# Performance work log

Measured on AMD Instinct MI355X. Metric: run time of the kernel, lower is better.

The kernel has to match this reference:

```python
import jax, jax.numpy as jnp
import numpy as np

MARGIN = 0.3
NEG_FALLBACK = 1e6  # value used when a row has no negatives


def setup_inputs() -> dict:
    key = jax.random.key(0)
    k1, k2 = jax.random.split(key)
    N, D, NUM_IDS = 8192, 256, 512
    feat = jax.random.normal(k1, (N, D), dtype=jnp.float32)
    labels = jax.random.randint(k2, (N,), 0, NUM_IDS, dtype=jnp.int64)
    return {"feat": feat, "labels": labels}


def reference(feat, labels):
    N = feat.shape[0]
    sq_norms = jnp.sum(feat * feat, axis=1)  # [N]
    sq = sq_norms[:, None] + sq_norms[None, :] - 2.0 * (feat @ feat.T)  # [N,N]
    sq = jnp.maximum(sq, 0.0)
    # safe sqrt (zero distance on the diagonal would otherwise give nan grads)
    dist = jnp.where(sq > 0, jnp.sqrt(jnp.where(sq > 0, sq, 1.0)), 0.0)

    same = labels[:, None] == labels[None, :]          # [N,N] bool
    eye = jnp.eye(N, dtype=bool)
    is_pos = same & ~eye                                # exclude self-pair
    is_neg = ~same

    # hard mining: per-row masked max over positives / min over negatives
    dist_ap = jnp.where(is_pos.any(axis=1),
                        jnp.where(is_pos, dist, -jnp.inf).max(axis=1), 0.0)
    dist_an = jnp.where(is_neg.any(axis=1),
                        jnp.where(is_neg, dist, jnp.inf).min(axis=1), NEG_FALLBACK)

    # MarginRankingLoss with y=1: mean(relu(margin - (dist_an - dist_ap)))
    return jnp.mean(jnp.maximum(0.0, MARGIN + dist_ap - dist_an))
```

## Files before the change

### kernel.cpp

```cpp
#include <hip/hip_runtime.h>


constexpr int N = 8192;
constexpr int D = 256;
constexpr float MARGIN = 0.3f;
constexpr float NEG_FALLBACK = 1e6f;
constexpr float TBIG = 1e30f;

typedef __attribute__((ext_vector_type(8))) __bf16 bf16x8;
typedef __attribute__((ext_vector_type(4))) float f32x4;

__device__ __forceinline__ unsigned enc_f(float f) {
  unsigned u = __float_as_uint(f);
  return (u >> 31) ? ~u : (u | 0x80000000u);
}
__device__ __forceinline__ float dec_f(unsigned e) {
  unsigned u = (e >> 31) ? (e ^ 0x80000000u) : ~e;
  return __uint_as_float(u);
}
__device__ __forceinline__ unsigned short f2bf_rtn(float x) {
  unsigned u = __float_as_uint(x);
  return (unsigned short)((u + 0x7fffu + ((u >> 16) & 1u)) >> 16);
}


__global__ __launch_bounds__(1024)
void tl_sortk(const int* __restrict__ labels, int* __restrict__ perm,
              int* __restrict__ labp, int* __restrict__ offg) {
  __shared__ int hist[512];
  __shared__ int wsum[8];
  __shared__ int wbase[8];
  const int tid = threadIdx.x;
  const int lane = tid & 63;
  const int w = tid >> 6;
  if (tid < 512) hist[tid] = 0;
  __syncthreads();
  int l8[8];
#pragma unroll
  for (int k = 0; k < 8; ++k) {
    l8[k] = labels[tid + k * 1024];
    atomicAdd(&hist[l8[k]], 1);
  }
  __syncthreads();
  int v = 0, sc = 0;
  if (tid < 512) {
    v = hist[tid];
    sc = v;
#pragma unroll
    for (int d = 1; d < 64; d <<= 1) {
      int t = __shfl_up(sc, d, 64);
      if (lane >= d) sc += t;
    }
    if (lane == 63) wsum[w] = sc;
  }
  __syncthreads();
  if (tid == 0) {
    int a = 0;
#pragma unroll
    for (int i = 0; i < 8; ++i) { wbase[i] = a; a += wsum[i]; }
  }
  __syncthreads();
  if (tid < 512) {
    const int excl = wbase[w] + sc - v;
    offg[tid] = excl;
    hist[tid] = excl;
  }
  if (tid == 0) offg[512] = N;
  __syncthreads();
#pragma unroll
  for (int k = 0; k < 8; ++k) {
    const int pos = atomicAdd(&hist[l8[k]], 1);
    perm[pos] = tid + k * 1024;
    labp[pos] = l8[k];
  }
}


__global__ void tl_pass0p(const float* __restrict__ feat, const int* __restrict__ perm,
                          float* __restrict__ norms, unsigned* __restrict__ ap,
                          unsigned* __restrict__ an, unsigned short* __restrict__ P,
                          float* __restrict__ out) {
  const int p = blockIdx.x * 4 + (threadIdx.x >> 6);
  const int lane = threadIdx.x & 63;
  const int src = perm[p];
  float4 f = reinterpret_cast<const float4*>(feat + (size_t)src * D)[lane];
  ushort4 h;
  h.x = f2bf_rtn(f.x); h.y = f2bf_rtn(f.y); h.z = f2bf_rtn(f.z); h.w = f2bf_rtn(f.w);
  reinterpret_cast<ushort4*>(P + (size_t)p * D)[lane] = h;
  float s = fmaf(f.x, f.x, fmaf(f.y, f.y, fmaf(f.z, f.z, f.w * f.w)));
#pragma unroll
  for (int off = 32; off > 0; off >>= 1) s += __shfl_down(s, off, 64);
  if (lane == 0) {
    norms[p] = s;
    ap[p] = enc_f(-TBIG);
    an[p] = enc_f(TBIG);
  }
  if (p == 0 && lane == 0) out[0] = 0.0f;
}


__global__ __launch_bounds__(512, 2)
void tl_pass1s(const unsigned short* __restrict__ P, const int* __restrict__ labp,
               const float* __restrict__ norms, const int* __restrict__ offg,
               unsigned* __restrict__ ap, unsigned* __restrict__ an) {
  __shared__ unsigned short lB[3][128][64];
  __shared__ float nrmS[512];
  __shared__ int lblS[512];

  const int tid = threadIdx.x;
  const int wave = tid >> 6;
  const int lane = tid & 63;
  const int c = lane & 15;
  const int q = lane >> 4;
  const int i0 = blockIdx.y * 256;
  const int j0 = blockIdx.x * 512;
  const int wrow = i0 + wave * 32;

  const int lo = offg[labp[i0]];
  const int hi = offg[labp[i0 + 255] + 1];

  const int rsub = lane >> 3;
  const int g7 = lane & 7;

#define STAGE(BUF, S1)                                                                  \
  do {                                                                                  \
    const int jb_ = j0 + ((S1) >> 2) * 128;                                             \
    const int kc_ = ((S1) & 3) * 64;                                                    \
    _Pragma("unroll") for (int t = 0; t < 2; ++t) {                                     \
      const int rA_ = wave * 16 + t * 8;                                                \
      const int sg_ = g7 ^ rsub;                                                        \
      const unsigned short* gp_ = P + (size_t)(jb_ + rA_ + rsub) * D + kc_ + sg_ * 8;   \
      __builtin_amdgcn_global_load_lds(                                                 \
          (const __attribute__((address_space(1))) void*)gp_,                           \
          (__attribute__((address_space(3))) void*)&lB[BUF][rA_][0], 16, 0, 0);         \
    }                                                                                   \
  } while (0)

#define WAITB2 do { asm volatile("s_waitcnt vmcnt(2)" ::: "memory"); \
                    __builtin_amdgcn_s_barrier(); } while (0)
#define WAITB0 do { asm volatile("s_waitcnt vmcnt(0)" ::: "memory"); \
                    __builtin_amdgcn_s_barrier(); } while (0)

  STAGE(0, 0);

  bf16x8 af[2][8];
#pragma unroll
  for (int a = 0; a < 2; ++a)
#pragma unroll
    for (int t2 = 0; t2 < 8; ++t2)
      af[a][t2] = *(const bf16x8*)(P + (size_t)(wrow + a * 16 + c) * D + t2 * 32 + q * 8);

  int lrow[2][4];
#pragma unroll
  for (int a = 0; a < 2; ++a)
#pragma unroll
    for (int r = 0; r < 4; ++r)
      lrow[a][r] = labp[wrow + a * 16 + q * 4 + r];

  nrmS[tid] = norms[j0 + tid];
  lblS[tid] = labp[j0 + tid];

  STAGE(1, 1);
  asm volatile("s_waitcnt vmcnt(2) lgkmcnt(0)" ::: "memory");
  __builtin_amdgcn_s_barrier();

  f32x4 acc[2][8];
#pragma unroll
  for (int a = 0; a < 2; ++a)
#pragma unroll
    for (int b = 0; b < 8; ++b) acc[a][b] = (f32x4){0.f, 0.f, 0.f, 0.f};

  float vp[2][4], vn[2][4];
#pragma unroll
  for (int a = 0; a < 2; ++a)
#pragma unroll
    for (int r = 0; r < 4; ++r) { vp[a][r] = -TBIG; vn[a][r] = TBIG; }

#pragma unroll
  for (int s = 0; s < 16; ++s) {
    const int jt = s >> 2;
    const int kk = s & 3;
    if (s + 2 < 16) STAGE((s + 2) % 3, s + 2);

#pragma unroll
    for (int ks = 0; ks < 2; ++ks) {
      const int gsel = ((ks * 4 + q) ^ (c & 7)) * 8;
      bf16x8 bfr[8];
#pragma unroll
      for (int b = 0; b < 8; ++b)
        bfr[b] = *(const bf16x8*)&lB[s % 3][b * 16 + c][gsel];
#pragma unroll
      for (int a = 0; a < 2; ++a)
#pragma unroll
        for (int b = 0; b < 8; ++b)
          acc[a][b] = __builtin_amdgcn_mfma_f32_16x16x32_bf16(
              af[a][kk * 2 + ks], bfr[b], acc[a][b], 0, 0, 0);
    }

    if (kk == 3) {
      const int jb0 = j0 + jt * 128;
      const int jls = jt * 128;
      const bool careful = (jb0 < hi) && (jb0 + 128 > lo);
      if (!careful) {
#pragma unroll
        for (int b = 0; b < 8; ++b) {
          const float njb = nrmS[jls + b * 16 + c];
#pragma unroll
          for (int a = 0; a < 2; ++a)
#pragma unroll
            for (int r = 0; r < 4; ++r)
              vn[a][r] = fminf(vn[a][r], fmaf(-2.f, acc[a][b][r], njb));
        }
      } else {
        int lj[8], cj[8];
        float nj[8];
#pragma unroll
        for (int b = 0; b < 8; ++b) {
          cj[b] = jb0 + b * 16 + c;
          nj[b] = nrmS[jls + b * 16 + c];
          lj[b] = lblS[jls + b * 16 + c];
        }
#pragma unroll
        for (int a = 0; a < 2; ++a)
#pragma unroll
          for (int r = 0; r < 4; ++r) {
            const int rg = wrow + a * 16 + q * 4 + r;
            const int li = lrow[a][r];
            float vpl = vp[a][r], vnl = vn[a][r];
#pragma unroll
            for (int b = 0; b < 8; ++b) {
              const float t = fmaf(-2.f, acc[a][b][r], nj[b]);
              const bool sm = (lj[b] == li);
              const bool dg = (cj[b] == rg);
              vpl = fmaxf(vpl, (sm && !dg) ? t : -TBIG);
              vnl = fminf(vnl, sm ? TBIG : t);
            }
            vp[a][r] = vpl;
            vn[a][r] = vnl;
          }
      }
#pragma unroll
      for (int a = 0; a < 2; ++a)
#pragma unroll
        for (int b = 0; b < 8; ++b) acc[a][b] = (f32x4){0.f, 0.f, 0.f, 0.f};
    }

    if (s < 14) {
      WAITB2;
    } else if (s == 14) {
      WAITB0;
    }
  }
#undef STAGE
#undef WAITB2
#undef WAITB0

#pragma unroll
  for (int a = 0; a < 2; ++a)
#pragma unroll
    for (int r = 0; r < 4; ++r) {
      float p = vp[a][r], n = vn[a][r];
#pragma unroll
      for (int m = 1; m < 16; m <<= 1) {
        p = fmaxf(p, __shfl_xor(p, m, 64));
        n = fminf(n, __shfl_xor(n, m, 64));
      }
      if (c == 0) {
        const int rg = wrow + a * 16 + q * 4 + r;
        atomicMax(&ap[rg], enc_f(p));
        atomicMin(&an[rg], enc_f(n));
      }
    }
}


__global__ void tl_pass2f(const unsigned* __restrict__ ap, const unsigned* __restrict__ an,
                          const float* __restrict__ norms, float* __restrict__ out) {
  int r = blockIdx.x * 256 + threadIdx.x;
  float ni = norms[r];
  float tpv = dec_f(ap[r]);
  float tnv = dec_f(an[r]);
  float dap = (tpv < -1e29f) ? 0.f : sqrtf(fmaxf(ni + tpv, 0.f));
  float dan = (tnv > 1e29f) ? NEG_FALLBACK : sqrtf(fmaxf(ni + tnv, 0.f));
  float v = fmaxf(0.f, MARGIN + dap - dan) * (1.0f / (float)N);
#pragma unroll
  for (int off = 32; off > 0; off >>= 1) v += __shfl_down(v, off, 64);
  __shared__ float red[4];
  int lane = threadIdx.x & 63, w = threadIdx.x >> 6;
  if (lane == 0) red[w] = v;
  __syncthreads();
  if (threadIdx.x == 0) atomicAdd(out, red[0] + red[1] + red[2] + red[3]);
}


constexpr int FB_BK = 32;
constexpr int FB_JSPLIT = 8;
constexpr int FB_JRANGE = N / FB_JSPLIT;
constexpr int FB_LDS = 132;

__global__ void tl_pass0_fb(const float* __restrict__ feat, float* __restrict__ norms,
                            float* __restrict__ ap, float* __restrict__ an,
                            float* __restrict__ out) {
  int row = blockIdx.x * 4 + (threadIdx.x >> 6);
  int lane = threadIdx.x & 63;
  float4 f = reinterpret_cast<const float4*>(feat + (size_t)row * D)[lane];
  float s = f.x * f.x + f.y * f.y + f.z * f.z + f.w * f.w;
#pragma unroll
  for (int off = 32; off > 0; off >>= 1) s += __shfl_down(s, off, 64);
  if (lane == 0) { norms[row] = s; ap[row] = 0.0f; an[row] = NEG_FALLBACK; }
  if (row == 0 && lane == 0) out[0] = 0.0f;
}

__global__ __launch_bounds__(256, 2)
void tl_pass1_fb(const float* __restrict__ feat, const int* __restrict__ labels,
                 const float* __restrict__ norms,
                 unsigned int* __restrict__ ap, unsigned int* __restrict__ an) {
  __shared__ float As[FB_BK][FB_LDS];
  __shared__ float Bs[FB_BK][FB_LDS];
  const int tid = threadIdx.x;
  const int tx = tid & 15, ty = tid >> 4;
  const int ib0 = blockIdx.y * 128;
  const int jbase = blockIdx.x * FB_JRANGE;
  float ni[8]; int li[8]; int ri[8];
#pragma unroll
  for (int a = 0; a < 8; ++a) {
    int r = ty * 4 + (a & 3) + ((a >> 2) << 6);
    ri[a] = ib0 + r; ni[a] = norms[ri[a]]; li[a] = labels[ri[a]];
  }
  float apv[8], anv[8];
#pragma unroll
  for (int a = 0; a < 8; ++a) { apv[a] = 0.0f; anv[a] = NEG_FALLBACK; }
  for (int jt = 0; jt < FB_JRANGE; jt += 128) {
    const int jb = jbase + jt;
    float acc[8][8];
#pragma unroll
    for (int a = 0; a < 8; ++a)
#pragma unroll
      for (int b = 0; b < 8; ++b) acc[a][b] = 0.0f;
    for (int kc = 0; kc < D; kc += FB_BK) {
#pragma unroll
      for (int u = 0; u < 4; ++u) {
        int lin = tid + u * 256;
        int row = lin >> 3, c4 = lin & 7;
        float4 va = *reinterpret_cast<const float4*>(feat + (size_t)(ib0 + row) * D + kc + c4 * 4);
        As[c4 * 4 + 0][row] = va.x; As[c4 * 4 + 1][row] = va.y;
        As[c4 * 4 + 2][row] = va.z; As[c4 * 4 + 3][row] = va.w;
        float4 vb = *reinterpret_cast<const float4*>(feat + (size_t)(jb + row) * D + kc + c4 * 4);
        Bs[c4 * 4 + 0][row] = vb.x; Bs[c4 * 4 + 1][row] = vb.y;
        Bs[c4 * 4 + 2][row] = vb.z; Bs[c4 * 4 + 3][row] = vb.w;
      }
      __syncthreads();
#pragma unroll 8
      for (int k = 0; k < FB_BK; ++k) {
        float4 a0 = *reinterpret_cast<const float4*>(&As[k][ty * 4]);
        float4 a1 = *reinterpret_cast<const float4*>(&As[k][64 + ty * 4]);
        float4 b0 = *reinterpret_cast<const float4*>(&Bs[k][tx * 4]);
        float4 b1 = *reinterpret_cast<const float4*>(&Bs[k][64 + tx * 4]);
        float av[8] = {a0.x, a0.y, a0.z, a0.w, a1.x, a1.y, a1.z, a1.w};
        float bv[8] = {b0.x, b0.y, b0.z, b0.w, b1.x, b1.y, b1.z, b1.w};
#pragma unroll
        for (int a = 0; a < 8; ++a)
#pragma unroll
          for (int b = 0; b < 8; ++b) acc[a][b] = fmaf(av[a], bv[b], acc[a][b]);
      }
      __syncthreads();
    }
#pragma unroll
    for (int b = 0; b < 8; ++b) {
      int cjx = jb + tx * 4 + (b & 3) + ((b >> 2) << 6);
      float njx = norms[cjx]; int ljx = labels[cjx];
#pragma unroll
      for (int a = 0; a < 8; ++a) {
        float sq = fmaxf(ni[a] + njx - 2.0f * acc[a][b], 0.0f);
        float dist = sqrtf(sq);
        if (li[a] == ljx) { if (ri[a] != cjx) apv[a] = fmaxf(apv[a], dist); }
        else anv[a] = fminf(anv[a], dist);
      }
    }
  }
  __syncthreads();
  float* red = &As[0][0];
#pragma unroll
  for (int a = 0; a < 8; ++a) {
    int r = ty * 4 + (a & 3) + ((a >> 2) << 6);
    red[r * 16 + tx] = apv[a];
  }
  __syncthreads();
  if (tid < 128) {
    float m = red[tid * 16];
#pragma unroll
    for (int t = 1; t < 16; ++t) m = fmaxf(m, red[tid * 16 + t]);
    atomicMax(&ap[ib0 + tid], __float_as_uint(m));
  }
  __syncthreads();
#pragma unroll
  for (int a = 0; a < 8; ++a) {
    int r = ty * 4 + (a & 3) + ((a >> 2) << 6);
    red[r * 16 + tx] = anv[a];
  }
  __syncthreads();
  if (tid < 128) {
    float m = red[tid * 16];
#pragma unroll
    for (int t = 1; t < 16; ++t) m = fminf(m, red[tid * 16 + t]);
    atomicMin(&an[ib0 + tid], __float_as_uint(m));
  }
}

__global__ void tl_pass2_fb(const float* __restrict__ ap, const float* __restrict__ an,
                            float* __restrict__ out) {
  int r = blockIdx.x * 256 + threadIdx.x;
  float v = fmaxf(0.0f, MARGIN + ap[r] - an[r]) * (1.0f / (float)N);
#pragma unroll
  for (int off = 32; off > 0; off >>= 1) v += __shfl_down(v, off, 64);
  __shared__ float red[4];
  int lane = threadIdx.x & 63, w = threadIdx.x >> 6;
  if (lane == 0) red[w] = v;
  __syncthreads();
  if (threadIdx.x == 0) atomicAdd(out, red[0] + red[1] + red[2] + red[3]);
}


extern "C" void kernel_launch(void* const* d_in, const int* in_sizes, int n_in,
                              void* d_out, int out_size, void* d_ws, size_t ws_size,
                              hipStream_t stream) {
  const float* feat = (const float*)d_in[0];
  const int* labels = (const int*)d_in[1];
  float* out = (float*)d_out;

  float* norms = (float*)d_ws;
  unsigned* ap = (unsigned*)(norms + N);
  unsigned* an = ap + N;
  int* perm = (int*)(an + N);
  int* labp = perm + N;
  int* offg = labp + N;
  unsigned short* P = (unsigned short*)(offg + 520);
  const size_t NEED = (size_t)5 * N * 4 + 520 * 4 + (size_t)N * D * 2;

  if (ws_size >= NEED) {
    tl_sortk<<<1, 1024, 0, stream>>>(labels, perm, labp, offg);
    tl_pass0p<<<N / 4, 256, 0, stream>>>(feat, perm, norms, ap, an, P, out);
    dim3 grid1(16, N / 256);
    tl_pass1s<<<grid1, 512, 0, stream>>>(P, labp, norms, offg, ap, an);
    tl_pass2f<<<N / 256, 256, 0, stream>>>(ap, an, norms, out);
  } else {
    float* apf = (float*)ap;
    float* anf = (float*)an;
    tl_pass0_fb<<<N / 4, 256, 0, stream>>>(feat, norms, apf, anf, out);
    dim3 grid1(FB_JSPLIT, N / 128);
    tl_pass1_fb<<<grid1, 256, 0, stream>>>(feat, labels, norms, (unsigned*)apf, (unsigned*)anf);
    tl_pass2_fb<<<N / 256, 256, 0, stream>>>(apf, anf, out);
  }
}
```

Baseline: 115.5 us.

## Interleave prefetch loads with MFMA sub-steps and raise priority during MFMA

Splits the two global-to-LDS prefetch loads of each stage across the two k-substeps, so each substep issues one load after reading its LDS fragments. Adds an extra barrier per substep, plus an explicit lgkmcnt wait and a sched_barrier before the MFMA block. Wraps the MFMAs in s_setprio(1) to favour matrix issue across waves, in a ping-pong style schedule. This adds twice as many barriers per stage, and the vmcnt accounting changes, which risks extra stalls or ordering problems.

After: 120.3 us. +4.2%, slower.

```diff
diff --git a/kernel.cpp b/kernel.cpp
--- a/kernel.cpp
+++ b/kernel.cpp
@@ -128,19 +128,14 @@
     const int kc_ = ((S1) & 3) * 64;                                                    \
     _Pragma("unroll") for (int t = 0; t < 2; ++t) {                                     \
       const int rA_ = wave * 16 + t * 8;                                                \
-      const int sg_ = g7 ^ rsub;                                                        \
-      const unsigned short* gp_ = P + (size_t)(jb_ + rA_ + rsub) * D + kc_ + sg_ * 8;   \
+      const unsigned short* gp_ =                                                       \
+          P + (size_t)(jb_ + rA_ + rsub) * D + kc_ + (g7 ^ rsub) * 8;                   \
       __builtin_amdgcn_global_load_lds(                                                 \
           (const __attribute__((address_space(1))) void*)gp_,                           \
           (__attribute__((address_space(3))) void*)&lB[BUF][rA_][0], 16, 0, 0);         \
     }                                                                                   \
   } while (0)
 
-#define WAITB2 do { asm volatile("s_waitcnt vmcnt(2)" ::: "memory"); \
-                    __builtin_amdgcn_s_barrier(); } while (0)
-#define WAITB0 do { asm volatile("s_waitcnt vmcnt(0)" ::: "memory"); \
-                    __builtin_amdgcn_s_barrier(); } while (0)
-
   STAGE(0, 0);
 
   bf16x8 af[2][8];
@@ -180,8 +175,6 @@
   for (int s = 0; s < 16; ++s) {
     const int jt = s >> 2;
     const int kk = s & 3;
-    if (s + 2 < 16) STAGE((s + 2) % 3, s + 2);
-
 #pragma unroll
     for (int ks = 0; ks < 2; ++ks) {
       const int gsel = ((ks * 4 + q) ^ (c & 7)) * 8;
@@ -189,71 +182,90 @@
 #pragma unroll
       for (int b = 0; b < 8; ++b)
         bfr[b] = *(const bf16x8*)&lB[s % 3][b * 16 + c][gsel];
+
+      if (s + 2 < 16) {
+        const int S1 = s + 2;
+        const int jb_ = j0 + (S1 >> 2) * 128;
+        const int kc_ = (S1 & 3) * 64;
+        const int rA_ = wave * 16 + ks * 8;
+        const unsigned short* gp_ =
+            P + (size_t)(jb_ + rA_ + rsub) * D + kc_ + (g7 ^ rsub) * 8;
+        __builtin_amdgcn_global_load_lds(
+            (const __attribute__((address_space(1))) void*)gp_,
+            (__attribute__((address_space(3))) void*)&lB[S1 % 3][rA_][0], 16, 0, 0);
+      }
+
+      __builtin_amdgcn_s_barrier();
+      asm volatile("s_waitcnt lgkmcnt(0)" ::: "memory");
+      __builtin_amdgcn_sched_barrier(0);
+
+      __builtin_amdgcn_s_setprio(1);
 #pragma unroll
       for (int a = 0; a < 2; ++a)
 #pragma unroll
         for (int b = 0; b < 8; ++b)
           acc[a][b] = __builtin_amdgcn_mfma_f32_16x16x32_bf16(
               af[a][kk * 2 + ks], bfr[b], acc[a][b], 0, 0, 0);
+      __builtin_amdgcn_s_setprio(0);
+
+      if (ks == 1) {
+        if (kk == 3) {
+          const int jb0 = j0 + jt * 128;
+          const int jls = jt * 128;
+          const bool careful = (jb0 < hi) && (jb0 + 128 > lo);
+          if (!careful) {
+#pragma unroll
+            for (int b = 0; b < 8; ++b) {
+              const float njb = nrmS[jls + b * 16 + c];
+#pragma unroll
+              for (int a = 0; a < 2; ++a)
+#pragma unroll
+                for (int r = 0; r < 4; ++r)
+                  vn[a][r] = fminf(vn[a][r], fmaf(-2.f, acc[a][b][r], njb));
+            }
+          } else {
+            int lj[8], cj[8];
+            float nj[8];
+#pragma unroll
+            for (int b = 0; b < 8; ++b) {
+              cj[b] = jb0 + b * 16 + c;
+              nj[b] = nrmS[jls + b * 16 + c];
+              lj[b] = lblS[jls + b * 16 + c];
+            }
+#pragma unroll
+            for (int a = 0; a < 2; ++a)
+#pragma unroll
+              for (int r = 0; r < 4; ++r) {
+                const int rg = wrow + a * 16 + q * 4 + r;
+                const int li = lrow[a][r];
+                float vpl = vp[a][r], vnl = vn[a][r];
+#pragma unroll
+                for (int b = 0; b < 8; ++b) {
+                  const float t = fmaf(-2.f, acc[a][b][r], nj[b]);
+                  const bool sm = (lj[b] == li);
+                  const bool dg = (cj[b] == rg);
+                  vpl = fmaxf(vpl, (sm && !dg) ? t : -TBIG);
+                  vnl = fminf(vnl, sm ? TBIG : t);
+                }
+                vp[a][r] = vpl;
+                vn[a][r] = vnl;
+              }
+          }
+#pragma unroll
+          for (int a = 0; a < 2; ++a)
+#pragma unroll
+            for (int b = 0; b < 8; ++b) acc[a][b] = (f32x4){0.f, 0.f, 0.f, 0.f};
+        }
+        if (s < 14) {
+          asm volatile("s_waitcnt vmcnt(2)" ::: "memory");
+        } else if (s == 14) {
+          asm volatile("s_waitcnt vmcnt(0)" ::: "memory");
+        }
+      }
+      __builtin_amdgcn_s_barrier();
     }
-
-    if (kk == 3) {
-      const int jb0 = j0 + jt * 128;
-      const int jls = jt * 128;
-      const bool careful = (jb0 < hi) && (jb0 + 128 > lo);
-      if (!careful) {
-#pragma unroll
-        for (int b = 0; b < 8; ++b) {
-          const float njb = nrmS[jls + b * 16 + c];
-#pragma unroll
-          for (int a = 0; a < 2; ++a)
-#pragma unroll
-            for (int r = 0; r < 4; ++r)
-              vn[a][r] = fminf(vn[a][r], fmaf(-2.f, acc[a][b][r], njb));
-        }
-      } else {
-        int lj[8], cj[8];
-        float nj[8];
-#pragma unroll
-        for (int b = 0; b < 8; ++b) {
-          cj[b] = jb0 + b * 16 + c;
-          nj[b] = nrmS[jls + b * 16 + c];
-          lj[b] = lblS[jls + b * 16 + c];
-        }
-#pragma unroll
-        for (int a = 0; a < 2; ++a)
-#pragma unroll
-          for (int r = 0; r < 4; ++r) {
-            const int rg = wrow + a * 16 + q * 4 + r;
-            const int li = lrow[a][r];
-            float vpl = vp[a][r], vnl = vn[a][r];
-#pragma unroll
-            for (int b = 0; b < 8; ++b) {
-              const float t = fmaf(-2.f, acc[a][b][r], nj[b]);
-              const bool sm = (lj[b] == li);
-              const bool dg = (cj[b] == rg);
-              vpl = fmaxf(vpl, (sm && !dg) ? t : -TBIG);
-              vnl = fminf(vnl, sm ? TBIG : t);
-            }
-            vp[a][r] = vpl;
-            vn[a][r] = vnl;
-          }
-      }
-#pragma unroll
-      for (int a = 0; a < 2; ++a)
-#pragma unroll
-        for (int b = 0; b < 8; ++b) acc[a][b] = (f32x4){0.f, 0.f, 0.f, 0.f};
-    }
-
-    if (s < 14) {
-      WAITB2;
-    } else if (s == 14) {
-      WAITB0;
-    }
   }
 #undef STAGE
-#undef WAITB2
-#undef WAITB0
 
 #pragma unroll
   for (int a = 0; a < 2; ++a)
```
